# Kernel optimization log

Measured on AMD Instinct MI355X. Metric: run time of the kernel, lower is better.

Reference implementation:

```python
import jax, jax.numpy as jnp
import numpy as np
import math

B, TQ, TK = 64, 1024, 512
CONV_CH, EMBED_DIM, ATT_HID = 512, 512, 512
KEY_POS_RATE = 1.385
QUERY_POS_RATE = 1.0
POSITION_WEIGHT = 1.0


def sin_pos_enc(positions, w, d):
    # positions: [B, T] int, padding_idx=0 maps to zero vector.
    # pe[..., 2i]   = sin(w*pos / 10000^(2i/d))
    # pe[..., 2i+1] = cos(w*pos / 10000^(2i/d))
    i = jnp.arange(d)
    inv_freq = jnp.power(jnp.float32(10000.0), -(2.0 * (i // 2).astype(jnp.float32)) / d)  # [d]
    ang = (positions.astype(jnp.float32) * w)[..., None] * inv_freq  # [B, T, d]
    pe = jnp.where(i % 2 == 0, jnp.sin(ang), jnp.cos(ang))
    return jnp.where((positions == 0)[..., None], jnp.float32(0.0), pe)


def setup_inputs() -> dict:
    key = jax.random.key(0)
    ks = jax.random.split(key, 12)
    s = 0.02
    inp = {
        "query": jax.random.normal(ks[0], (B, TQ, CONV_CH), jnp.float32),
        "keys": jax.random.normal(ks[1], (B, TK, EMBED_DIM), jnp.float32),
        "values": jax.random.normal(ks[2], (B, TK, EMBED_DIM), jnp.float32),
        # 1-based positions (0 is the padding index of SinusoidalEncoding)
        "text_positions": jnp.broadcast_to(jnp.arange(1, TK + 1, dtype=jnp.int64), (B, TK)),
        "frame_positions": jnp.broadcast_to(jnp.arange(1, TQ + 1, dtype=jnp.int64), (B, TQ)),
        # pad mask over keys: last 64 text positions are padding
        "mask": jnp.broadcast_to(jnp.arange(TK) >= (TK - 64), (B, TK)),
        "Wq": jax.random.normal(ks[3], (CONV_CH, ATT_HID), jnp.float32) * s,
        "bq": jnp.zeros((ATT_HID,), jnp.float32),
        "Wk": jax.random.normal(ks[4], (EMBED_DIM, ATT_HID), jnp.float32) * s,
        "bk": jnp.zeros((ATT_HID,), jnp.float32),
        "Wv": jax.random.normal(ks[5], (EMBED_DIM, ATT_HID), jnp.float32) * s,
        "bv": jnp.zeros((ATT_HID,), jnp.float32),
        "Wo": jax.random.normal(ks[6], (ATT_HID, CONV_CH), jnp.float32) * s,
        "bo": jnp.zeros((CONV_CH,), jnp.float32),
    }
    return inp


def reference(query, keys, values, text_positions, frame_positions, mask,
              Wq, bq, Wk, bk, Wv, bv, Wo, bo):
    # positional-bias injection (position_weight = 1.0)
    keys = keys + POSITION_WEIGHT * sin_pos_enc(text_positions, KEY_POS_RATE, EMBED_DIM)[:, :keys.shape[1], :]
    query = query + POSITION_WEIGHT * sin_pos_enc(frame_positions, QUERY_POS_RATE, CONV_CH)[:, :frame_positions.shape[-1], :]

    v = values @ Wv + bv            # [B, TK, H]
    k = keys @ Wk + bk              # [B, TK, H]
    q = query @ Wq + bq             # [B, TQ, H]

    scores = jnp.einsum('bqh,bkh->bqk', q, k)               # [B, TQ, TK]
    scores = jnp.where(mask[:, None, :], -jnp.inf, scores)
    attn = jax.nn.softmax(scores, axis=2)
    # dropout is a no-op in eval mode
    x = jnp.einsum('bqk,bkh->bqh', attn, v)
    x = x * jnp.float32(math.sqrt(1.0 / v.shape[1]))
    out = x @ Wo + bo               # [B, TQ, conv_channels]
    return out, attn
```

## Files before the change

### kernel.cpp

```cpp
#include <hip/hip_runtime.h>
#include <stdint.h>

#define DEVI __device__ __forceinline__

typedef __attribute__((ext_vector_type(4))) float     f4v;
typedef __attribute__((ext_vector_type(8))) _Float16  h8;
typedef __attribute__((ext_vector_type(4))) _Float16  h4;
typedef unsigned int  u32;

static constexpr int   TQ = 1024, TKN = 512;
static constexpr float KEY_RATE = 1.385f;
static constexpr float QRY_RATE = 1.0f;
static constexpr float SCALE    = 0.04419417382415922f;
static constexpr float INVC     = 0.05190512648261504f;

static constexpr size_t OFF_MM   = 0;
static constexpr size_t OFF_NT   = OFF_MM  + (size_t)512*512*2;
static constexpr size_t OFF_WOT  = OFF_NT  + (size_t)512*512*2;
static constexpr size_t OFF_PEQ  = OFF_WOT + (size_t)512*512*4;
static constexpr size_t OFF_W    = OFF_PEQ + (size_t)1024*512*4;
static constexpr size_t OFF_C    = OFF_W   + 512*4;
static constexpr size_t OFF_BQBK = OFF_C   + 512*4;
static constexpr size_t OFF_T    = OFF_BQBK + 256;
static constexpr size_t OFF_KP   = OFF_T   + (size_t)64*512*4;
static constexpr size_t OFF_MKT  = OFF_KP  + (size_t)64*512*512*2;
static constexpr size_t OFF_PT   = OFF_MKT + (size_t)64*512*512*2;
static constexpr size_t WS_NEED  = OFF_PT  + (size_t)64*512*512*2;
static constexpr size_t OFF_A16  = WS_NEED;
static constexpr size_t WS_BIG   = OFF_A16 + (size_t)64*1024*512*2;

DEVI f4v mfma16(h8 a, h8 b, f4v c) {
  return __builtin_amdgcn_mfma_f32_16x16x32_f16(a, b, c, 0, 0, 0);
}

DEVI void gld16(void* lds, const void* g) {
  __builtin_amdgcn_global_load_lds(
      (const __attribute__((address_space(1))) unsigned int*)g,
      (__attribute__((address_space(3))) unsigned int*)lds, 16, 0, 0);
}

DEVI void stage_B(char* Bbuf, const _Float16* B, int k0, int tid) {
#pragma unroll
  for (int it = 0; it < 4; ++it) {
    const int c = (it << 9) + tid;
    const int r = c >> 2, s = c & 3;
    const int sg = s ^ ((r >> 1) & 3);
    gld16(Bbuf + ((size_t)c << 4), B + (size_t)r * 512 + k0 + (sg << 3));
  }
}

DEVI void stage_A16(char* Abuf, const _Float16* A, int k0, int tid) {
  const int r = tid >> 2, s = tid & 3;
  const int sg = s ^ ((r >> 1) & 3);
  gld16(Abuf + ((size_t)tid << 4), A + (size_t)r * 512 + k0 + (sg << 3));
}

DEVI void loads_A32(f4v& x0, f4v& x1, const float* A, const float* add, int k0, int tid) {
  const int r = tid >> 2, c8 = (tid & 3) << 3;
  const float* p = A + (size_t)r * 512 + k0 + c8;
  x0 = *(const f4v*)p; x1 = *(const f4v*)(p + 4);
  if (add) {
    const float* q = add + (size_t)r * 512 + k0 + c8;
    x0 += *(const f4v*)q; x1 += *(const f4v*)(q + 4);
  }
}
DEVI void write_A32(char* Abuf, f4v x0, f4v x1, int tid) {
  const int r = tid >> 2;
  const int slot = (tid & 3) ^ ((r >> 1) & 3);
  h8 o;
#pragma unroll
  for (int i = 0; i < 4; ++i) { o[i] = (_Float16)x0[i]; o[4 + i] = (_Float16)x1[i]; }
  *(h8*)(Abuf + (r << 6) + (slot << 4)) = o;
}

DEVI void read_frags(const char* Ab, const char* Bb, int wr, int wc, int lane,
                     h8 (&a)[4], h8 (&b)[8]) {
  const int l15 = lane & 15, hi = lane >> 4;
#pragma unroll
  for (int mi = 0; mi < 4; ++mi) {
    const int r = wr * 64 + mi * 16 + l15;
    a[mi] = *(const h8*)(Ab + (r << 6) + ((hi ^ ((r >> 1) & 3)) << 4));
  }
#pragma unroll
  for (int nj = 0; nj < 8; ++nj) {
    const int g = wc * 128 + nj * 16 + l15;
    b[nj] = *(const h8*)(Bb + (g << 6) + ((hi ^ ((g >> 1) & 3)) << 4));
  }
}

#define MFMA_ALL(a, bf, acc)                                   \
  _Pragma("unroll") for (int mi = 0; mi < 4; ++mi)             \
  _Pragma("unroll") for (int nj = 0; nj < 8; ++nj)             \
      acc[mi][nj] = mfma16(a[mi], bf[nj], acc[mi][nj]);

DEVI void stage_f32_A(char* Abuf, const float* A, int k0, int tid) {
#pragma unroll
  for (int it = 0; it < 2; ++it) {
    const int idx = (it << 9) + tid;
    const int r = idx >> 3, c4 = idx & 7;
    f4v x = *(const f4v*)(A + (size_t)r * 512 + k0 + (c4 << 2));
    h4 o;
#pragma unroll
    for (int i = 0; i < 4; ++i) o[i] = (_Float16)x[i];
    const int slot = (c4 >> 1) ^ ((r >> 1) & 3);
    *(h4*)(Abuf + (r << 6) + (slot << 4) + ((c4 & 1) << 3)) = o;
  }
}
DEVI void stage_f32_B(char* Bbuf, const float* B, int k0, int tid) {
#pragma unroll
  for (int it = 0; it < 8; ++it) {
    const int idx = (it << 9) + tid;
    const int r = idx >> 3, c4 = idx & 7;
    f4v x = *(const f4v*)(B + (size_t)r * 512 + k0 + (c4 << 2));
    h4 o;
#pragma unroll
    for (int i = 0; i < 4; ++i) o[i] = (_Float16)x[i];
    const int slot = (c4 >> 1) ^ ((r >> 1) & 3);
    *(h4*)(Bbuf + (r << 6) + (slot << 4) + ((c4 & 1) << 3)) = o;
  }
}

__global__ __launch_bounds__(512) void k_prep_small(
    const float* __restrict__ Wk, const float* __restrict__ bq,
    const float* __restrict__ bk, const float* __restrict__ bv,
    const float* __restrict__ Wo, const float* __restrict__ bo,
    float* __restrict__ wvec, float* __restrict__ cvec, float* __restrict__ bqbk) {
  __shared__ float red[512];
  const int tid = threadIdx.x, wid = tid >> 6, lane = tid & 63;
  if (blockIdx.x < 64) {
    const int row = blockIdx.x * 8 + wid;
    const float* p = Wk + (size_t)row * 512 + lane * 8;
    const f4v a = *(const f4v*)p, c = *(const f4v*)(p + 4);
    const f4v b0 = *(const f4v*)(bq + lane * 8), b1 = *(const f4v*)(bq + lane * 8 + 4);
    float d = a[0]*b0[0]+a[1]*b0[1]+a[2]*b0[2]+a[3]*b0[3]
            + c[0]*b1[0]+c[1]*b1[1]+c[2]*b1[2]+c[3]*b1[3];
#pragma unroll
    for (int off = 32; off; off >>= 1) d += __shfl_xor(d, off);
    if (lane == 0) wvec[row] = d;
  } else {
    float acc = 0.f;
    for (int a = 0; a < 512; ++a) acc += bv[a] * Wo[(size_t)a * 512 + tid];
    cvec[tid] = SCALE * acc + bo[tid];
    red[tid] = bq[tid] * bk[tid];
    __syncthreads();
    if (tid == 0) { float s = 0.f; for (int h = 0; h < 512; ++h) s += red[h]; bqbk[0] = s; }
  }
}

__global__ void k_prep_peq(const void* __restrict__ fpos_raw, float* __restrict__ PEQ) {
  const u32* fp = (const u32*)fpos_raw;
  const bool is64 = (fp[1] == 0);
  const int t  = blockIdx.x * 256 + threadIdx.x;
  const int tq = t >> 9, d = t & 511;
  const int pos = (int)(is64 ? fp[2 * tq] : fp[tq]);
  float pe = 0.f;
  if (pos != 0) {
    const float invf = exp2f(-(float)(d >> 1) * INVC);
    const float ang  = ((float)pos * QRY_RATE) * invf;
    pe = (d & 1) ? cosf(ang) : sinf(ang);
  }
  PEQ[t] = pe;
}

__global__ __launch_bounds__(256) void k_wo_t(const float* __restrict__ Wo,
                                              float* __restrict__ WoT) {
  __shared__ float t[32][33];
  const int tx = threadIdx.x, ty = threadIdx.y;
  const int x = blockIdx.x * 32 + tx;
#pragma unroll
  for (int j = 0; j < 4; ++j)
    t[ty + 8 * j][tx] = Wo[(size_t)(blockIdx.y * 32 + ty + 8 * j) * 512 + x];
  __syncthreads();
  const int x2 = blockIdx.y * 32 + tx;
#pragma unroll
  for (int j = 0; j < 4; ++j)
    WoT[(size_t)(blockIdx.x * 32 + ty + 8 * j) * 512 + x2] = t[tx][ty + 8 * j];
}

__global__ __launch_bounds__(512) void k_prep_mats(
    const float* __restrict__ Wq, const float* __restrict__ Wk,
    const float* __restrict__ WoT, const float* __restrict__ Wv,
    _Float16* __restrict__ Mm, _Float16* __restrict__ Nt) {
  __shared__ char lds[40960];
  char *Ab = lds, *Bb = lds + 8192;
  const int tid = threadIdx.x, lane = tid & 63, wid = tid >> 6;
  const int wr = wid >> 2, wc = wid & 3;
  const float* A = (blockIdx.y == 0 ? Wq : WoT) + (size_t)blockIdx.x * 128 * 512;
  const float* B = (blockIdx.y == 0 ? Wk : Wv);
  _Float16* out = (blockIdx.y == 0 ? Mm : Nt) + (size_t)blockIdx.x * 128 * 512;
  f4v acc[4][8] = {};
  for (int ks = 0; ks < 16; ++ks) {
    stage_f32_A(Ab, A, ks * 32, tid);
    stage_f32_B(Bb, B, ks * 32, tid);
    __syncthreads();
    h8 a[4], bf[8];
    read_frags(Ab, Bb, wr, wc, lane, a, bf);
    MFMA_ALL(a, bf, acc);
    __syncthreads();
  }
  const int l15 = lane & 15, hi = lane >> 4;
#pragma unroll
  for (int mi = 0; mi < 4; ++mi)
#pragma unroll
    for (int nj = 0; nj < 8; ++nj) {
      const int col = wc * 128 + nj * 16 + l15;
#pragma unroll
      for (int j = 0; j < 4; ++j) {
        const int row = wr * 64 + mi * 16 + hi * 4 + j;
        out[(size_t)row * 512 + col] = (_Float16)acc[mi][nj][j];
      }
    }
}

__global__ __launch_bounds__(256) void k_prep_keys(
    const float* __restrict__ keys, const void* __restrict__ tpos_raw,
    const void* __restrict__ mask_raw,
    const float* __restrict__ wvec, const float* __restrict__ bqbk,
    _Float16* __restrict__ kp, float* __restrict__ tvec) {
  const u32* tp = (const u32*)tpos_raw;
  const bool is64 = (tp[1] == 0);
  const int tid = threadIdx.x, wid = tid >> 6, lane = tid & 63;
  const int row = blockIdx.x * 4 + wid;
  const int pos = (int)(is64 ? tp[2 * row] : tp[row]);
  const int d0  = lane * 8;
  const float* src = keys + (size_t)row * 512 + d0;
  const f4v a = *(const f4v*)src, b = *(const f4v*)(src + 4);
  float x[8] = {a[0], a[1], a[2], a[3], b[0], b[1], b[2], b[3]};
  if (pos != 0) {
    const float pw = (float)pos * KEY_RATE;
#pragma unroll
    for (int u = 0; u < 4; ++u) {
      const float invf = exp2f(-(float)(lane * 4 + u) * INVC);
      const float ang  = pw * invf;
      x[2*u]   += sinf(ang);
      x[2*u+1] += cosf(ang);
    }
  }
  const f4v w0 = *(const f4v*)(wvec + d0), w1 = *(const f4v*)(wvec + d0 + 4);
  float dot = 0.f;
#pragma unroll
  for (int i = 0; i < 4; ++i) dot += x[i] * w0[i] + x[4+i] * w1[i];
#pragma unroll
  for (int off = 32; off; off >>= 1) dot += __shfl_xor(dot, off);
  if (lane == 0) {
    const u32* m32 = (const u32*)mask_raw;
    const bool is32 = (m32[448] != 0);
    const bool mk = is32 ? (m32[row] != 0)
                         : (((const unsigned char*)mask_raw)[row] != 0);
    tvec[row] = mk ? -1e30f : (dot + bqbk[0]);
  }
  h8 o;
#pragma unroll
  for (int i = 0; i < 8; ++i) o[i] = (_Float16)x[i];
  *(h8*)(kp + (size_t)row * 512 + d0) = o;
}


__global__ __launch_bounds__(512, 2) void k_mk(
    const _Float16* __restrict__ kp, const _Float16* __restrict__ Mm,
    _Float16* __restrict__ MKt) {
  __shared__ char lds[81920];
  char *Ac = lds, *An = lds + 8192, *Bc = lds + 16384, *Bn = lds + 49152;
  const int tid = threadIdx.x, lane = tid & 63, wid = tid >> 6;
  const int wr = wid >> 2, wc = wid & 3;
  const int tt = blockIdx.x, b = blockIdx.y;
  const _Float16* As = kp + ((size_t)b * TKN + tt * 128) * 512;
  f4v acc[4][8] = {};
  stage_A16(Ac, As, 0, tid);
  stage_B(Bc, Mm, 0, tid);
  __syncthreads();
  for (int ks = 0; ks < 16; ++ks) {
    if (ks < 15) { stage_A16(An, As, (ks + 1) * 32, tid); stage_B(Bn, Mm, (ks + 1) * 32, tid); }
    h8 a[4], bf[8];
    read_frags(Ac, Bc, wr, wc, lane, a, bf);
    MFMA_ALL(a, bf, acc);
    __syncthreads();
    char* t = Ac; Ac = An; An = t; t = Bc; Bc = Bn; Bn = t;
  }
  _Float16* Ob = MKt + (size_t)b * TKN * 512 + (size_t)tt * 128 * 512;
  const int l15 = lane & 15, hi = lane >> 4;
#pragma unroll
  for (int mi = 0; mi < 4; ++mi)
#pragma unroll
    for (int nj = 0; nj < 8; ++nj) {
      const int col = wc * 128 + nj * 16 + l15;
#pragma unroll
      for (int j = 0; j < 4; ++j) {
        const int row = wr * 64 + mi * 16 + hi * 4 + j;
        Ob[(size_t)row * 512 + col] = (_Float16)acc[mi][nj][j];
      }
    }
}

__global__ __launch_bounds__(512, 2) void k_scores(
    const float* __restrict__ query, const float* __restrict__ PEQ,
    const _Float16* __restrict__ MKt, const float* __restrict__ tve,
    float* __restrict__ attn, _Float16* __restrict__ a16) {
  __shared__ char lds[81920];
  char *Ac = lds, *An = lds + 8192, *Bc = lds + 16384, *Bn = lds + 49152;
  const int tid = threadIdx.x, lane = tid & 63, wid = tid >> 6;
  const int wr = wid >> 2, wc = wid & 3;
  const int qt = blockIdx.x, b = blockIdx.y;
  const float* As = query + ((size_t)b * TQ + qt * 128) * 512;
  const float* Ad = PEQ + (size_t)(qt * 128) * 512;
  const _Float16* Bs = MKt + (size_t)b * TKN * 512;
  const int l15 = lane & 15, hi = lane >> 4;
  float tv[8];
#pragma unroll
  for (int nj = 0; nj < 8; ++nj) tv[nj] = tve[b * TKN + wc * 128 + nj * 16 + l15];
  f4v acc[4][8] = {};
  f4v x0, x1;
  loads_A32(x0, x1, As, Ad, 0, tid);
  stage_B(Bc, Bs, 0, tid);
  write_A32(Ac, x0, x1, tid);
  __syncthreads();
  for (int ks = 0; ks < 16; ++ks) {
    if (ks < 15) { loads_A32(x0, x1, As, Ad, (ks + 1) * 32, tid); stage_B(Bn, Bs, (ks + 1) * 32, tid); }
    h8 a[4], bf[8];
    read_frags(Ac, Bc, wr, wc, lane, a, bf);
    MFMA_ALL(a, bf, acc);
    if (ks < 15) write_A32(An, x0, x1, tid);
    __syncthreads();
    char* t = Ac; Ac = An; An = t; t = Bc; Bc = Bn; Bn = t;
  }
  float* red  = (float*)lds;
  float* red2 = (float*)(lds + 2048);
#pragma unroll
  for (int mi = 0; mi < 4; ++mi)
#pragma unroll
    for (int nj = 0; nj < 8; ++nj) {
      const float t = tv[nj];
#pragma unroll
      for (int j = 0; j < 4; ++j) acc[mi][nj][j] += t;
    }
  float mrow[4][4];
#pragma unroll
  for (int mi = 0; mi < 4; ++mi)
#pragma unroll
    for (int j = 0; j < 4; ++j) {
      float m = acc[mi][0][j];
#pragma unroll
      for (int nj = 1; nj < 8; ++nj) m = fmaxf(m, acc[mi][nj][j]);
      m = fmaxf(m, __shfl_xor(m, 1)); m = fmaxf(m, __shfl_xor(m, 2));
      m = fmaxf(m, __shfl_xor(m, 4)); m = fmaxf(m, __shfl_xor(m, 8));
      mrow[mi][j] = m;
    }
  if (l15 == 0) {
#pragma unroll
    for (int mi = 0; mi < 4; ++mi)
#pragma unroll
      for (int j = 0; j < 4; ++j)
        red[(wr * 64 + mi * 16 + hi * 4 + j) * 4 + wc] = mrow[mi][j];
  }
  __syncthreads();
#pragma unroll
  for (int mi = 0; mi < 4; ++mi)
#pragma unroll
    for (int j = 0; j < 4; ++j) {
      const f4v rv = *(const f4v*)(red + (wr * 64 + mi * 16 + hi * 4 + j) * 4);
      mrow[mi][j] = fmaxf(fmaxf(rv[0], rv[1]), fmaxf(rv[2], rv[3]));
    }
  float srow[4][4];
#pragma unroll
  for (int mi = 0; mi < 4; ++mi)
#pragma unroll
    for (int j = 0; j < 4; ++j) {
      float s = 0.f;
      const float m = mrow[mi][j];
#pragma unroll
      for (int nj = 0; nj < 8; ++nj) {
        const float e = expf(acc[mi][nj][j] - m);
        acc[mi][nj][j] = e; s += e;
      }
      s += __shfl_xor(s, 1); s += __shfl_xor(s, 2);
      s += __shfl_xor(s, 4); s += __shfl_xor(s, 8);
      srow[mi][j] = s;
    }
  if (l15 == 0) {
#pragma unroll
    for (int mi = 0; mi < 4; ++mi)
#pragma unroll
      for (int j = 0; j < 4; ++j)
        red2[(wr * 64 + mi * 16 + hi * 4 + j) * 4 + wc] = srow[mi][j];
  }
  __syncthreads();
  float* Ao = attn + ((size_t)b * TQ + qt * 128) * 512;
  _Float16* Ah = a16 ? a16 + ((size_t)b * TQ + qt * 128) * 512 : nullptr;
#pragma unroll
  for (int mi = 0; mi < 4; ++mi)
#pragma unroll
    for (int j = 0; j < 4; ++j) {
      const int row = wr * 64 + mi * 16 + hi * 4 + j;
      const f4v sv = *(const f4v*)(red2 + row * 4);
      const float rinv = 1.f / (sv[0] + sv[1] + sv[2] + sv[3]);
#pragma unroll
      for (int nj = 0; nj < 8; ++nj) {
        const float v = acc[mi][nj][j] * rinv;
        const int col = wc * 128 + nj * 16 + l15;
        Ao[(size_t)row * 512 + col] = v;
        if (Ah) Ah[(size_t)row * 512 + col] = (_Float16)v;
      }
    }
}

__global__ __launch_bounds__(512, 2) void k_pv(
    const float* __restrict__ values, const _Float16* __restrict__ Nt,
    _Float16* __restrict__ Pt) {
  __shared__ char lds[81920];
  char *Ac = lds, *An = lds + 8192, *Bc = lds + 16384, *Bn = lds + 49152;
  const int tid = threadIdx.x, lane = tid & 63, wid = tid >> 6;
  const int wr = wid >> 2, wc = wid & 3;
  const int rt = blockIdx.x, b = blockIdx.y;
  const float* As = values + ((size_t)b * TKN + rt * 128) * 512;
  f4v acc[4][8] = {};
  f4v x0, x1;
  loads_A32(x0, x1, As, nullptr, 0, tid);
  stage_B(Bc, Nt, 0, tid);
  write_A32(Ac, x0, x1, tid);
  __syncthreads();
  for (int ks = 0; ks < 16; ++ks) {
    if (ks < 15) { loads_A32(x0, x1, As, nullptr, (ks + 1) * 32, tid); stage_B(Bn, Nt, (ks + 1) * 32, tid); }
    h8 a[4], bf[8];
    read_frags(Ac, Bc, wr, wc, lane, a, bf);
    MFMA_ALL(a, bf, acc);
    if (ks < 15) write_A32(An, x0, x1, tid);
    __syncthreads();
    char* t = Ac; Ac = An; An = t; t = Bc; Bc = Bn; Bn = t;
  }
  const int l15 = lane & 15, hi = lane >> 4;
  _Float16* Pb = Pt + (size_t)b * 512 * 512;
#pragma unroll
  for (int mi = 0; mi < 4; ++mi)
#pragma unroll
    for (int nj = 0; nj < 8; ++nj) {
      const int col = wc * 128 + nj * 16 + l15;
      const int t0  = rt * 128 + wr * 64 + mi * 16 + hi * 4;
      h4 o;
#pragma unroll
      for (int j = 0; j < 4; ++j) o[j] = (_Float16)acc[mi][nj][j];
      *(h4*)(Pb + (size_t)col * 512 + t0) = o;
    }
}

template <int A16P>
__global__ __launch_bounds__(512, 2) void k_final(
    const float* __restrict__ attn, const _Float16* __restrict__ attn16,
    const _Float16* __restrict__ Pt, const float* __restrict__ cvec,
    float* __restrict__ outp) {
  __shared__ char lds[81920];
  char *Ac = lds, *An = lds + 8192, *Bc = lds + 16384, *Bn = lds + 49152;
  const int tid = threadIdx.x, lane = tid & 63, wid = tid >> 6;
  const int wr = wid >> 2, wc = wid & 3;
  const int qt = blockIdx.x, b = blockIdx.y;
  const float* As = attn + ((size_t)b * TQ + qt * 128) * 512;
  const _Float16* As16 = attn16 + ((size_t)b * TQ + qt * 128) * 512;
  const _Float16* Bs = Pt + (size_t)b * 512 * 512;
  const int l15 = lane & 15, hi = lane >> 4;
  float cv[8];
#pragma unroll
  for (int nj = 0; nj < 8; ++nj) cv[nj] = cvec[wc * 128 + nj * 16 + l15];
  f4v acc[4][8] = {};
  f4v x0, x1;
  if (A16P) {
    stage_A16(Ac, As16, 0, tid);
  } else {
    loads_A32(x0, x1, As, nullptr, 0, tid);
  }
  stage_B(Bc, Bs, 0, tid);
  if (!A16P) write_A32(Ac, x0, x1, tid);
  __syncthreads();
  for (int ks = 0; ks < 16; ++ks) {
    if (ks < 15) {
      if (A16P) stage_A16(An, As16, (ks + 1) * 32, tid);
      else      loads_A32(x0, x1, As, nullptr, (ks + 1) * 32, tid);
      stage_B(Bn, Bs, (ks + 1) * 32, tid);
    }
    h8 a[4], bf[8];
    read_frags(Ac, Bc, wr, wc, lane, a, bf);
    MFMA_ALL(a, bf, acc);
    if (!A16P && ks < 15) write_A32(An, x0, x1, tid);
    __syncthreads();
    char* t = Ac; Ac = An; An = t; t = Bc; Bc = Bn; Bn = t;
  }
  float* Ob = outp + ((size_t)b * TQ + qt * 128) * 512;
#pragma unroll
  for (int mi = 0; mi < 4; ++mi)
#pragma unroll
    for (int nj = 0; nj < 8; ++nj) {
      const int col = wc * 128 + nj * 16 + l15;
#pragma unroll
      for (int j = 0; j < 4; ++j) {
        const int row = wr * 64 + mi * 16 + hi * 4 + j;
        Ob[(size_t)row * 512 + col] = SCALE * acc[mi][nj][j] + cv[nj];
      }
    }
}

extern "C" void kernel_launch(void* const* d_in, const int* in_sizes, int n_in,
                              void* d_out, int out_size, void* d_ws, size_t ws_size,
                              hipStream_t stream) {
  (void)in_sizes; (void)n_in; (void)out_size;
  if (ws_size < WS_NEED) return;
  const bool big = (ws_size >= WS_BIG);

  const float* query  = (const float*)d_in[0];
  const float* keys   = (const float*)d_in[1];
  const float* values = (const float*)d_in[2];
  const void*  tpos   = d_in[3];
  const void*  fpos   = d_in[4];
  const void*  mask   = d_in[5];
  const float* Wq = (const float*)d_in[6];
  const float* bq = (const float*)d_in[7];
  const float* Wk = (const float*)d_in[8];
  const float* bk = (const float*)d_in[9];
  const float* Wv = (const float*)d_in[10];
  const float* bv = (const float*)d_in[11];
  const float* Wo = (const float*)d_in[12];
  const float* bo = (const float*)d_in[13];

  char* ws = (char*)d_ws;
  _Float16* Mm   = (_Float16*)(ws + OFF_MM);
  _Float16* Nt   = (_Float16*)(ws + OFF_NT);
  float*    WoT  = (float*)   (ws + OFF_WOT);
  float*    PEQ  = (float*)   (ws + OFF_PEQ);
  float*    wvec = (float*)   (ws + OFF_W);
  float*    cvec = (float*)   (ws + OFF_C);
  float*    bqbk = (float*)   (ws + OFF_BQBK);
  float*    tvec = (float*)   (ws + OFF_T);
  _Float16* kp   = (_Float16*)(ws + OFF_KP);
  _Float16* MKt  = (_Float16*)(ws + OFF_MKT);
  _Float16* Pt   = (_Float16*)(ws + OFF_PT);
  _Float16* a16  = big ? (_Float16*)(ws + OFF_A16) : nullptr;

  float* outp = (float*)d_out;
  float* attn = outp + (size_t)64 * TQ * 512;

  k_prep_small<<<65, 512, 0, stream>>>(Wk, bq, bk, bv, Wo, bo, wvec, cvec, bqbk);
  k_prep_peq  <<<2048, 256, 0, stream>>>(fpos, PEQ);
  k_wo_t      <<<dim3(16, 16), dim3(32, 8), 0, stream>>>(Wo, WoT);
  k_prep_mats <<<dim3(4, 2), 512, 0, stream>>>(Wq, Wk, WoT, Wv, Mm, Nt);
  k_prep_keys <<<8192, 256, 0, stream>>>(keys, tpos, mask, wvec, bqbk, kp, tvec);
  k_mk        <<<dim3(4, 64), 512, 0, stream>>>(kp, Mm, MKt);
  k_scores    <<<dim3(8, 64), 512, 0, stream>>>(query, PEQ, MKt, tvec, attn, a16);
  k_pv        <<<dim3(4, 64), 512, 0, stream>>>(values, Nt, Pt);
  if (big) k_final<1><<<dim3(8, 64), 512, 0, stream>>>(attn, a16, Pt, cvec, outp);
  else     k_final<0><<<dim3(8, 64), 512, 0, stream>>>(attn, a16, Pt, cvec, outp);
}
```

Measured before the change: 359.6 us.

## Fuse softmax and PV into one attention kernel, merge prep launches

Merges the scores kernel with the final attn@P GEMM so the normalized probabilities are kept in registers, written to LDS as fp16, and multiplied by Pt in the same block. This removes the re-read of the fp32 attention matrix (or its fp16 copy) from global memory and the separate final launch. It also collapses the small prep kernels into two launches, merges the MK and PV GEMMs into one grid, and maps blocks to batches with an XCD-aware interleave. The cost is higher LDS use per block (96KB), which may cut occupancy, plus serialized per-column-tile writes of P into LDS with extra barriers.

```diff
diff --git a/kernel.cpp b/kernel.cpp
--- a/kernel.cpp
+++ b/kernel.cpp
@@ -26,8 +26,6 @@
 static constexpr size_t OFF_MKT  = OFF_KP  + (size_t)64*512*512*2;
 static constexpr size_t OFF_PT   = OFF_MKT + (size_t)64*512*512*2;
 static constexpr size_t WS_NEED  = OFF_PT  + (size_t)64*512*512*2;
-static constexpr size_t OFF_A16  = WS_NEED;
-static constexpr size_t WS_BIG   = OFF_A16 + (size_t)64*1024*512*2;
 
 DEVI f4v mfma16(h8 a, h8 b, f4v c) {
   return __builtin_amdgcn_mfma_f32_16x16x32_f16(a, b, c, 0, 0, 0);
@@ -73,18 +71,28 @@
   *(h8*)(Abuf + (r << 6) + (slot << 4)) = o;
 }
 
-DEVI void read_frags(const char* Ab, const char* Bb, int wr, int wc, int lane,
-                     h8 (&a)[4], h8 (&b)[8]) {
+DEVI void read_fragsA(const char* Ab, int wr, int lane, h8 (&a)[4]) {
   const int l15 = lane & 15, hi = lane >> 4;
 #pragma unroll
   for (int mi = 0; mi < 4; ++mi) {
     const int r = wr * 64 + mi * 16 + l15;
     a[mi] = *(const h8*)(Ab + (r << 6) + ((hi ^ ((r >> 1) & 3)) << 4));
   }
+}
+DEVI void read_fragsB(const char* Bb, int wc, int lane, h8 (&b)[8]) {
+  const int l15 = lane & 15, hi = lane >> 4;
 #pragma unroll
   for (int nj = 0; nj < 8; ++nj) {
     const int g = wc * 128 + nj * 16 + l15;
     b[nj] = *(const h8*)(Bb + (g << 6) + ((hi ^ ((g >> 1) & 3)) << 4));
+  }
+}
+DEVI void read_fragsP(const char* Pb, int kt, int wr, int lane, h8 (&a)[4]) {
+  const int l15 = lane & 15, hi = lane >> 4;
+#pragma unroll
+  for (int mi = 0; mi < 4; ++mi) {
+    const int r = wr * 64 + mi * 16 + l15;
+    a[mi] = *(const h8*)(Pb + r * 256 + (kt << 6) + ((hi ^ ((r >> 1) & 3)) << 4));
   }
 }
 
@@ -120,15 +128,17 @@
   }
 }
 
-__global__ __launch_bounds__(512) void k_prep_small(
+__global__ __launch_bounds__(256) void k_prepA(
     const float* __restrict__ Wk, const float* __restrict__ bq,
     const float* __restrict__ bk, const float* __restrict__ bv,
     const float* __restrict__ Wo, const float* __restrict__ bo,
-    float* __restrict__ wvec, float* __restrict__ cvec, float* __restrict__ bqbk) {
-  __shared__ float red[512];
-  const int tid = threadIdx.x, wid = tid >> 6, lane = tid & 63;
-  if (blockIdx.x < 64) {
-    const int row = blockIdx.x * 8 + wid;
+    const void* __restrict__ fpos_raw,
+    float* __restrict__ wvec, float* __restrict__ cvec, float* __restrict__ bqbk,
+    float* __restrict__ PEQ, float* __restrict__ WoT) {
+  const int bid = blockIdx.x, tid = threadIdx.x;
+  if (bid < 128) {
+    const int wid = tid >> 6, lane = tid & 63;
+    const int row = bid * 4 + wid;
     const float* p = Wk + (size_t)row * 512 + lane * 8;
     const f4v a = *(const f4v*)p, c = *(const f4v*)(p + 4);
     const f4v b0 = *(const f4v*)(bq + lane * 8), b1 = *(const f4v*)(bq + lane * 8 + 4);
@@ -137,194 +147,241 @@
 #pragma unroll
     for (int off = 32; off; off >>= 1) d += __shfl_xor(d, off);
     if (lane == 0) wvec[row] = d;
+  } else if (bid == 128) {
+    __shared__ float red[256];
+#pragma unroll
+    for (int u = 0; u < 2; ++u) {
+      const int i = tid + u * 256;
+      float acc = 0.f;
+      for (int a = 0; a < 512; ++a) acc += bv[a] * Wo[(size_t)a * 512 + i];
+      cvec[i] = SCALE * acc + bo[i];
+    }
+    red[tid] = bq[tid] * bk[tid] + bq[tid + 256] * bk[tid + 256];
+    __syncthreads();
+    if (tid == 0) { float s = 0.f; for (int h = 0; h < 256; ++h) s += red[h]; bqbk[0] = s; }
+  } else if (bid < 129 + 2048) {
+    const u32* fp = (const u32*)fpos_raw;
+    const bool is64 = (fp[1] == 0);
+    const int t = (bid - 129) * 256 + tid;
+    const int tq = t >> 9, d = t & 511;
+    const int pos = (int)(is64 ? fp[2 * tq] : fp[tq]);
+    float pe = 0.f;
+    if (pos != 0) {
+      const float invf = exp2f(-(float)(d >> 1) * INVC);
+      const float ang  = ((float)pos * QRY_RATE) * invf;
+      pe = (d & 1) ? cosf(ang) : sinf(ang);
+    }
+    PEQ[t] = pe;
   } else {
-    float acc = 0.f;
-    for (int a = 0; a < 512; ++a) acc += bv[a] * Wo[(size_t)a * 512 + tid];
-    cvec[tid] = SCALE * acc + bo[tid];
-    red[tid] = bq[tid] * bk[tid];
-    __syncthreads();
-    if (tid == 0) { float s = 0.f; for (int h = 0; h < 512; ++h) s += red[h]; bqbk[0] = s; }
-  }
-}
-
-__global__ void k_prep_peq(const void* __restrict__ fpos_raw, float* __restrict__ PEQ) {
-  const u32* fp = (const u32*)fpos_raw;
-  const bool is64 = (fp[1] == 0);
-  const int t  = blockIdx.x * 256 + threadIdx.x;
-  const int tq = t >> 9, d = t & 511;
-  const int pos = (int)(is64 ? fp[2 * tq] : fp[tq]);
-  float pe = 0.f;
-  if (pos != 0) {
-    const float invf = exp2f(-(float)(d >> 1) * INVC);
-    const float ang  = ((float)pos * QRY_RATE) * invf;
-    pe = (d & 1) ? cosf(ang) : sinf(ang);
-  }
-  PEQ[t] = pe;
-}
-
-__global__ __launch_bounds__(256) void k_wo_t(const float* __restrict__ Wo,
-                                              float* __restrict__ WoT) {
-  __shared__ float t[32][33];
-  const int tx = threadIdx.x, ty = threadIdx.y;
-  const int x = blockIdx.x * 32 + tx;
-#pragma unroll
-  for (int j = 0; j < 4; ++j)
-    t[ty + 8 * j][tx] = Wo[(size_t)(blockIdx.y * 32 + ty + 8 * j) * 512 + x];
-  __syncthreads();
-  const int x2 = blockIdx.y * 32 + tx;
-#pragma unroll
-  for (int j = 0; j < 4; ++j)
-    WoT[(size_t)(blockIdx.x * 32 + ty + 8 * j) * 512 + x2] = t[tx][ty + 8 * j];
-}
-
-__global__ __launch_bounds__(512) void k_prep_mats(
+    __shared__ float t[32][33];
+    const int local = bid - 2177;
+    const int bx = local & 15, by = local >> 4;
+    const int tx = tid & 31, ty = tid >> 5;
+    const int x = bx * 32 + tx;
+#pragma unroll
+    for (int j = 0; j < 4; ++j)
+      t[ty + 8 * j][tx] = Wo[(size_t)(by * 32 + ty + 8 * j) * 512 + x];
+    __syncthreads();
+    const int x2 = by * 32 + tx;
+#pragma unroll
+    for (int j = 0; j < 4; ++j)
+      WoT[(size_t)(bx * 32 + ty + 8 * j) * 512 + x2] = t[tx][ty + 8 * j];
+  }
+}
+
+__global__ __launch_bounds__(512) void k_prepB(
     const float* __restrict__ Wq, const float* __restrict__ Wk,
     const float* __restrict__ WoT, const float* __restrict__ Wv,
-    _Float16* __restrict__ Mm, _Float16* __restrict__ Nt) {
-  __shared__ char lds[40960];
-  char *Ab = lds, *Bb = lds + 8192;
-  const int tid = threadIdx.x, lane = tid & 63, wid = tid >> 6;
-  const int wr = wid >> 2, wc = wid & 3;
-  const float* A = (blockIdx.y == 0 ? Wq : WoT) + (size_t)blockIdx.x * 128 * 512;
-  const float* B = (blockIdx.y == 0 ? Wk : Wv);
-  _Float16* out = (blockIdx.y == 0 ? Mm : Nt) + (size_t)blockIdx.x * 128 * 512;
-  f4v acc[4][8] = {};
-  for (int ks = 0; ks < 16; ++ks) {
-    stage_f32_A(Ab, A, ks * 32, tid);
-    stage_f32_B(Bb, B, ks * 32, tid);
-    __syncthreads();
-    h8 a[4], bf[8];
-    read_frags(Ab, Bb, wr, wc, lane, a, bf);
-    MFMA_ALL(a, bf, acc);
-    __syncthreads();
-  }
-  const int l15 = lane & 15, hi = lane >> 4;
-#pragma unroll
-  for (int mi = 0; mi < 4; ++mi)
-#pragma unroll
-    for (int nj = 0; nj < 8; ++nj) {
-      const int col = wc * 128 + nj * 16 + l15;
-#pragma unroll
-      for (int j = 0; j < 4; ++j) {
-        const int row = wr * 64 + mi * 16 + hi * 4 + j;
-        out[(size_t)row * 512 + col] = (_Float16)acc[mi][nj][j];
-      }
-    }
-}
-
-__global__ __launch_bounds__(256) void k_prep_keys(
     const float* __restrict__ keys, const void* __restrict__ tpos_raw,
     const void* __restrict__ mask_raw,
     const float* __restrict__ wvec, const float* __restrict__ bqbk,
+    _Float16* __restrict__ Mm, _Float16* __restrict__ Nt,
     _Float16* __restrict__ kp, float* __restrict__ tvec) {
-  const u32* tp = (const u32*)tpos_raw;
-  const bool is64 = (tp[1] == 0);
-  const int tid = threadIdx.x, wid = tid >> 6, lane = tid & 63;
-  const int row = blockIdx.x * 4 + wid;
-  const int pos = (int)(is64 ? tp[2 * row] : tp[row]);
-  const int d0  = lane * 8;
-  const float* src = keys + (size_t)row * 512 + d0;
-  const f4v a = *(const f4v*)src, b = *(const f4v*)(src + 4);
-  float x[8] = {a[0], a[1], a[2], a[3], b[0], b[1], b[2], b[3]};
-  if (pos != 0) {
-    const float pw = (float)pos * KEY_RATE;
-#pragma unroll
-    for (int u = 0; u < 4; ++u) {
-      const float invf = exp2f(-(float)(lane * 4 + u) * INVC);
-      const float ang  = pw * invf;
-      x[2*u]   += sinf(ang);
-      x[2*u+1] += cosf(ang);
-    }
-  }
-  const f4v w0 = *(const f4v*)(wvec + d0), w1 = *(const f4v*)(wvec + d0 + 4);
-  float dot = 0.f;
-#pragma unroll
-  for (int i = 0; i < 4; ++i) dot += x[i] * w0[i] + x[4+i] * w1[i];
-#pragma unroll
-  for (int off = 32; off; off >>= 1) dot += __shfl_xor(dot, off);
-  if (lane == 0) {
-    const u32* m32 = (const u32*)mask_raw;
-    const bool is32 = (m32[448] != 0);
-    const bool mk = is32 ? (m32[row] != 0)
-                         : (((const unsigned char*)mask_raw)[row] != 0);
-    tvec[row] = mk ? -1e30f : (dot + bqbk[0]);
-  }
-  h8 o;
-#pragma unroll
-  for (int i = 0; i < 8; ++i) o[i] = (_Float16)x[i];
-  *(h8*)(kp + (size_t)row * 512 + d0) = o;
-}
-
-
-__global__ __launch_bounds__(512, 2) void k_mk(
+  __shared__ char lds[40960];
+  const int bid = blockIdx.x, tid = threadIdx.x;
+  const int lane = tid & 63, wid = tid >> 6;
+  if (bid < 8) {
+    char *Ab = lds, *Bb = lds + 8192;
+    const int wr = wid >> 2, wc = wid & 3;
+    const int x = bid & 3, y = bid >> 2;
+    const float* A = (y == 0 ? Wq : WoT) + (size_t)x * 128 * 512;
+    const float* B = (y == 0 ? Wk : Wv);
+    _Float16* out = (y == 0 ? Mm : Nt) + (size_t)x * 128 * 512;
+    f4v acc[4][8] = {};
+    for (int ks = 0; ks < 16; ++ks) {
+      stage_f32_A(Ab, A, ks * 32, tid);
+      stage_f32_B(Bb, B, ks * 32, tid);
+      __syncthreads();
+      h8 a[4], bf[8];
+      read_fragsA(Ab, wr, lane, a);
+      read_fragsB(Bb, wc, lane, bf);
+      MFMA_ALL(a, bf, acc);
+      __syncthreads();
+    }
+    const int l15 = lane & 15, hi = lane >> 4;
+#pragma unroll
+    for (int mi = 0; mi < 4; ++mi)
+#pragma unroll
+      for (int nj = 0; nj < 8; ++nj) {
+        const int col = wc * 128 + nj * 16 + l15;
+#pragma unroll
+        for (int j = 0; j < 4; ++j) {
+          const int row = wr * 64 + mi * 16 + hi * 4 + j;
+          out[(size_t)row * 512 + col] = (_Float16)acc[mi][nj][j];
+        }
+      }
+  } else {
+    const u32* tp = (const u32*)tpos_raw;
+    const bool is64 = (tp[1] == 0);
+    const int row = (bid - 8) * 8 + wid;
+    const int pos = (int)(is64 ? tp[2 * row] : tp[row]);
+    const int d0  = lane * 8;
+    const float* src = keys + (size_t)row * 512 + d0;
+    const f4v a = *(const f4v*)src, b = *(const f4v*)(src + 4);
+    float x[8] = {a[0], a[1], a[2], a[3], b[0], b[1], b[2], b[3]};
+    if (pos != 0) {
+      const float pw = (float)pos * KEY_RATE;
+#pragma unroll
+      for (int u = 0; u < 4; ++u) {
+        const float invf = exp2f(-(float)(lane * 4 + u) * INVC);
+        const float ang  = pw * invf;
+        x[2*u]   += sinf(ang);
+        x[2*u+1] += cosf(ang);
+      }
+    }
+    const f4v w0 = *(const f4v*)(wvec + d0), w1 = *(const f4v*)(wvec + d0 + 4);
+    float dot = 0.f;
+#pragma unroll
+    for (int i = 0; i < 4; ++i) dot += x[i] * w0[i] + x[4+i] * w1[i];
+#pragma unroll
+    for (int off = 32; off; off >>= 1) dot += __shfl_xor(dot, off);
+    if (lane == 0) {
+      const u32* m32 = (const u32*)mask_raw;
+      const bool is32 = (m32[448] != 0);
+      const bool mk = is32 ? (m32[row] != 0)
+                           : (((const unsigned char*)mask_raw)[row] != 0);
+      tvec[row] = mk ? -1e30f : (dot + bqbk[0]);
+    }
+    h8 o;
+#pragma unroll
+    for (int i = 0; i < 8; ++i) o[i] = (_Float16)x[i];
+    *(h8*)(kp + (size_t)row * 512 + d0) = o;
+  }
+}
+
+__global__ __launch_bounds__(512, 2) void k_mkpv(
     const _Float16* __restrict__ kp, const _Float16* __restrict__ Mm,
-    _Float16* __restrict__ MKt) {
+    const float* __restrict__ values, const _Float16* __restrict__ Nt,
+    _Float16* __restrict__ MKt, _Float16* __restrict__ Pt) {
   __shared__ char lds[81920];
   char *Ac = lds, *An = lds + 8192, *Bc = lds + 16384, *Bn = lds + 49152;
+  const int bid = blockIdx.x, tid = threadIdx.x;
+  const int lane = tid & 63, wid = tid >> 6;
+  const int wr = wid >> 2, wc = wid & 3;
+  const int l15 = lane & 15, hi = lane >> 4;
+  f4v acc[4][8] = {};
+  if (bid < 256) {
+    const int tt = bid & 3, b = bid >> 2;
+    const _Float16* As = kp + ((size_t)b * TKN + tt * 128) * 512;
+    stage_A16(Ac, As, 0, tid);
+    stage_B(Bc, Mm, 0, tid);
+    __syncthreads();
+    for (int ks = 0; ks < 16; ++ks) {
+      if (ks < 15) { stage_A16(An, As, (ks + 1) * 32, tid); stage_B(Bn, Mm, (ks + 1) * 32, tid); }
+      h8 a[4], bf[8];
+      read_fragsA(Ac, wr, lane, a);
+      read_fragsB(Bc, wc, lane, bf);
+      MFMA_ALL(a, bf, acc);
+      __syncthreads();
+      char* t = Ac; Ac = An; An = t; t = Bc; Bc = Bn; Bn = t;
+    }
+    _Float16* Ob = MKt + (size_t)b * TKN * 512 + (size_t)tt * 128 * 512;
+#pragma unroll
+    for (int mi = 0; mi < 4; ++mi)
+#pragma unroll
+      for (int nj = 0; nj < 8; ++nj) {
+        const int col = wc * 128 + nj * 16 + l15;
+#pragma unroll
+        for (int j = 0; j < 4; ++j) {
+          const int row = wr * 64 + mi * 16 + hi * 4 + j;
+          Ob[(size_t)row * 512 + col] = (_Float16)acc[mi][nj][j];
+        }
+      }
+  } else {
+    const int rt = (bid - 256) & 3, b = (bid - 256) >> 2;
+    const float* As = values + ((size_t)b * TKN + rt * 128) * 512;
+    f4v x0, x1;
+    loads_A32(x0, x1, As, nullptr, 0, tid);
+    stage_B(Bc, Nt, 0, tid);
+    write_A32(Ac, x0, x1, tid);
+    __syncthreads();
+    for (int ks = 0; ks < 16; ++ks) {
+      if (ks < 15) { loads_A32(x0, x1, As, nullptr, (ks + 1) * 32, tid); stage_B(Bn, Nt, (ks + 1) * 32, tid); }
+      h8 a[4], bf[8];
+      read_fragsA(Ac, wr, lane, a);
+      read_fragsB(Bc, wc, lane, bf);
+      MFMA_ALL(a, bf, acc);
+      if (ks < 15) write_A32(An, x0, x1, tid);
+      __syncthreads();
+      char* t = Ac; Ac = An; An = t; t = Bc; Bc = Bn; Bn = t;
+    }
+    _Float16* Pb = Pt + (size_t)b * 512 * 512;
+#pragma unroll
+    for (int mi = 0; mi < 4; ++mi)
+#pragma unroll
+      for (int nj = 0; nj < 8; ++nj) {
+        const int col = wc * 128 + nj * 16 + l15;
+        const int t0  = rt * 128 + wr * 64 + mi * 16 + hi * 4;
+        h4 o;
+#pragma unroll
+        for (int j = 0; j < 4; ++j) o[j] = (_Float16)acc[mi][nj][j];
+        *(h4*)(Pb + (size_t)col * 512 + t0) = o;
+      }
+  }
+}
+
+__global__ __launch_bounds__(512, 2) void k_att(
+    const float* __restrict__ query, const float* __restrict__ PEQ,
+    const _Float16* __restrict__ MKt, const float* __restrict__ tve,
+    const _Float16* __restrict__ Pt, const float* __restrict__ cvec,
+    float* __restrict__ attn, float* __restrict__ outp) {
+  __shared__ char lds[98304];
+  char *A0 = lds, *A1 = lds + 8192, *B0 = lds + 16384, *B1 = lds + 49152;
+  float* red  = (float*)(lds + 81920);
+  float* red2 = (float*)(lds + 83968);
+  const int bid = blockIdx.x;
+  const int xcd = bid & 7, jj = bid >> 3;
+  const int b = xcd + 8 * (jj & 7), qt = jj >> 3;
   const int tid = threadIdx.x, lane = tid & 63, wid = tid >> 6;
   const int wr = wid >> 2, wc = wid & 3;
-  const int tt = blockIdx.x, b = blockIdx.y;
-  const _Float16* As = kp + ((size_t)b * TKN + tt * 128) * 512;
-  f4v acc[4][8] = {};
-  stage_A16(Ac, As, 0, tid);
-  stage_B(Bc, Mm, 0, tid);
-  __syncthreads();
-  for (int ks = 0; ks < 16; ++ks) {
-    if (ks < 15) { stage_A16(An, As, (ks + 1) * 32, tid); stage_B(Bn, Mm, (ks + 1) * 32, tid); }
-    h8 a[4], bf[8];
-    read_frags(Ac, Bc, wr, wc, lane, a, bf);
-    MFMA_ALL(a, bf, acc);
-    __syncthreads();
-    char* t = Ac; Ac = An; An = t; t = Bc; Bc = Bn; Bn = t;
-  }
-  _Float16* Ob = MKt + (size_t)b * TKN * 512 + (size_t)tt * 128 * 512;
   const int l15 = lane & 15, hi = lane >> 4;
-#pragma unroll
-  for (int mi = 0; mi < 4; ++mi)
-#pragma unroll
-    for (int nj = 0; nj < 8; ++nj) {
-      const int col = wc * 128 + nj * 16 + l15;
-#pragma unroll
-      for (int j = 0; j < 4; ++j) {
-        const int row = wr * 64 + mi * 16 + hi * 4 + j;
-        Ob[(size_t)row * 512 + col] = (_Float16)acc[mi][nj][j];
-      }
-    }
-}
-
-__global__ __launch_bounds__(512, 2) void k_scores(
-    const float* __restrict__ query, const float* __restrict__ PEQ,
-    const _Float16* __restrict__ MKt, const float* __restrict__ tve,
-    float* __restrict__ attn, _Float16* __restrict__ a16) {
-  __shared__ char lds[81920];
-  char *Ac = lds, *An = lds + 8192, *Bc = lds + 16384, *Bn = lds + 49152;
-  const int tid = threadIdx.x, lane = tid & 63, wid = tid >> 6;
-  const int wr = wid >> 2, wc = wid & 3;
-  const int qt = blockIdx.x, b = blockIdx.y;
   const float* As = query + ((size_t)b * TQ + qt * 128) * 512;
   const float* Ad = PEQ + (size_t)(qt * 128) * 512;
   const _Float16* Bs = MKt + (size_t)b * TKN * 512;
-  const int l15 = lane & 15, hi = lane >> 4;
+  const _Float16* PtB = Pt + (size_t)b * 512 * 512;
   float tv[8];
 #pragma unroll
   for (int nj = 0; nj < 8; ++nj) tv[nj] = tve[b * TKN + wc * 128 + nj * 16 + l15];
+
   f4v acc[4][8] = {};
   f4v x0, x1;
   loads_A32(x0, x1, As, Ad, 0, tid);
-  stage_B(Bc, Bs, 0, tid);
-  write_A32(Ac, x0, x1, tid);
+  stage_B(B0, Bs, 0, tid);
+  write_A32(A0, x0, x1, tid);
   __syncthreads();
+  char *Ac = A0, *An = A1, *Bc = B0, *Bn = B1;
   for (int ks = 0; ks < 16; ++ks) {
     if (ks < 15) { loads_A32(x0, x1, As, Ad, (ks + 1) * 32, tid); stage_B(Bn, Bs, (ks + 1) * 32, tid); }
     h8 a[4], bf[8];
-    read_frags(Ac, Bc, wr, wc, lane, a, bf);
+    read_fragsA(Ac, wr, lane, a);
+    read_fragsB(Bc, wc, lane, bf);
     MFMA_ALL(a, bf, acc);
     if (ks < 15) write_A32(An, x0, x1, tid);
     __syncthreads();
     char* t = Ac; Ac = An; An = t; t = Bc; Bc = Bn; Bn = t;
   }
-  float* red  = (float*)lds;
-  float* red2 = (float*)(lds + 2048);
+  stage_B(lds + 32768, PtB, 0, tid);
+
 #pragma unroll
   for (int mi = 0; mi < 4; ++mi)
 #pragma unroll
@@ -384,8 +441,9 @@
         red2[(wr * 64 + mi * 16 + hi * 4 + j) * 4 + wc] = srow[mi][j];
   }
   __syncthreads();
+
   float* Ao = attn + ((size_t)b * TQ + qt * 128) * 512;
-  _Float16* Ah = a16 ? a16 + ((size_t)b * TQ + qt * 128) * 512 : nullptr;
+  h4 pk[4][8];
 #pragma unroll
   for (int mi = 0; mi < 4; ++mi)
 #pragma unroll
@@ -396,102 +454,52 @@
 #pragma unroll
       for (int nj = 0; nj < 8; ++nj) {
         const float v = acc[mi][nj][j] * rinv;
-        const int col = wc * 128 + nj * 16 + l15;
-        Ao[(size_t)row * 512 + col] = v;
-        if (Ah) Ah[(size_t)row * 512 + col] = (_Float16)v;
-      }
-    }
-}
-
-__global__ __launch_bounds__(512, 2) void k_pv(
-    const float* __restrict__ values, const _Float16* __restrict__ Nt,
-    _Float16* __restrict__ Pt) {
-  __shared__ char lds[81920];
-  char *Ac = lds, *An = lds + 8192, *Bc = lds + 16384, *Bn = lds + 49152;
-  const int tid = threadIdx.x, lane = tid & 63, wid = tid >> 6;
-  const int wr = wid >> 2, wc = wid & 3;
-  const int rt = blockIdx.x, b = blockIdx.y;
-  const float* As = values + ((size_t)b * TKN + rt * 128) * 512;
-  f4v acc[4][8] = {};
-  f4v x0, x1;
-  loads_A32(x0, x1, As, nullptr, 0, tid);
-  stage_B(Bc, Nt, 0, tid);
-  write_A32(Ac, x0, x1, tid);
-  __syncthreads();
-  for (int ks = 0; ks < 16; ++ks) {
-    if (ks < 15) { loads_A32(x0, x1, As, nullptr, (ks + 1) * 32, tid); stage_B(Bn, Nt, (ks + 1) * 32, tid); }
-    h8 a[4], bf[8];
-    read_frags(Ac, Bc, wr, wc, lane, a, bf);
-    MFMA_ALL(a, bf, acc);
-    if (ks < 15) write_A32(An, x0, x1, tid);
-    __syncthreads();
-    char* t = Ac; Ac = An; An = t; t = Bc; Bc = Bn; Bn = t;
-  }
-  const int l15 = lane & 15, hi = lane >> 4;
-  _Float16* Pb = Pt + (size_t)b * 512 * 512;
+        Ao[(size_t)row * 512 + wc * 128 + nj * 16 + l15] = v;
+        pk[mi][nj][j] = (_Float16)v;
+      }
+    }
+
+  f4v oacc[4][8] = {};
+  char* Pl = lds;
+  for (int ct = 0; ct < 4; ++ct) {
+    __syncthreads();
+    if (wc == ct) {
+#pragma unroll
+      for (int mi = 0; mi < 4; ++mi)
+#pragma unroll
+        for (int nj = 0; nj < 8; ++nj)
+#pragma unroll
+          for (int j = 0; j < 4; ++j) {
+            const int r = wr * 64 + mi * 16 + hi * 4 + j;
+            const int cc = (((nj & 1) << 1) | (l15 >> 3)) ^ ((r >> 1) & 3);
+            *(_Float16*)(Pl + r * 256 + ((nj >> 1) << 6) + (cc << 4) + ((l15 & 7) << 1)) =
+                pk[mi][nj][j];
+          }
+    }
+    __syncthreads();
+    for (int kt = 0; kt < 4; ++kt) {
+      const int s = ct * 4 + kt;
+      if (s < 15) stage_B(lds + 32768 + (((s + 1) & 1) << 15), PtB, (s + 1) * 32, tid);
+      h8 a[4], bb[8];
+      read_fragsP(Pl, kt, wr, lane, a);
+      read_fragsB(lds + 32768 + ((s & 1) << 15), wc, lane, bb);
+      MFMA_ALL(a, bb, oacc);
+      if (kt < 3) __syncthreads();
+    }
+  }
+  float cv[8];
+#pragma unroll
+  for (int nj = 0; nj < 8; ++nj) cv[nj] = cvec[wc * 128 + nj * 16 + l15];
+  float* Ob = outp + ((size_t)b * TQ + qt * 128) * 512;
 #pragma unroll
   for (int mi = 0; mi < 4; ++mi)
 #pragma unroll
     for (int nj = 0; nj < 8; ++nj) {
       const int col = wc * 128 + nj * 16 + l15;
-      const int t0  = rt * 128 + wr * 64 + mi * 16 + hi * 4;
-      h4 o;
-#pragma unroll
-      for (int j = 0; j < 4; ++j) o[j] = (_Float16)acc[mi][nj][j];
-      *(h4*)(Pb + (size_t)col * 512 + t0) = o;
-    }
-}
-
-template <int A16P>
-__global__ __launch_bounds__(512, 2) void k_final(
-    const float* __restrict__ attn, const _Float16* __restrict__ attn16,
-    const _Float16* __restrict__ Pt, const float* __restrict__ cvec,
-    float* __restrict__ outp) {
-  __shared__ char lds[81920];
-  char *Ac = lds, *An = lds + 8192, *Bc = lds + 16384, *Bn = lds + 49152;
-  const int tid = threadIdx.x, lane = tid & 63, wid = tid >> 6;
-  const int wr = wid >> 2, wc = wid & 3;
-  const int qt = blockIdx.x, b = blockIdx.y;
-  const float* As = attn + ((size_t)b * TQ + qt * 128) * 512;
-  const _Float16* As16 = attn16 + ((size_t)b * TQ + qt * 128) * 512;
-  const _Float16* Bs = Pt + (size_t)b * 512 * 512;
-  const int l15 = lane & 15, hi = lane >> 4;
-  float cv[8];
-#pragma unroll
-  for (int nj = 0; nj < 8; ++nj) cv[nj] = cvec[wc * 128 + nj * 16 + l15];
-  f4v acc[4][8] = {};
-  f4v x0, x1;
-  if (A16P) {
-    stage_A16(Ac, As16, 0, tid);
-  } else {
-    loads_A32(x0, x1, As, nullptr, 0, tid);
-  }
-  stage_B(Bc, Bs, 0, tid);
-  if (!A16P) write_A32(Ac, x0, x1, tid);
-  __syncthreads();
-  for (int ks = 0; ks < 16; ++ks) {
-    if (ks < 15) {
-      if (A16P) stage_A16(An, As16, (ks + 1) * 32, tid);
-      else      loads_A32(x0, x1, As, nullptr, (ks + 1) * 32, tid);
-      stage_B(Bn, Bs, (ks + 1) * 32, tid);
-    }
-    h8 a[4], bf[8];
-    read_frags(Ac, Bc, wr, wc, lane, a, bf);
-    MFMA_ALL(a, bf, acc);
-    if (!A16P && ks < 15) write_A32(An, x0, x1, tid);
-    __syncthreads();
-    char* t = Ac; Ac = An; An = t; t = Bc; Bc = Bn; Bn = t;
-  }
-  float* Ob = outp + ((size_t)b * TQ + qt * 128) * 512;
-#pragma unroll
-  for (int mi = 0; mi < 4; ++mi)
-#pragma unroll
-    for (int nj = 0; nj < 8; ++nj) {
-      const int col = wc * 128 + nj * 16 + l15;
 #pragma unroll
       for (int j = 0; j < 4; ++j) {
         const int row = wr * 64 + mi * 16 + hi * 4 + j;
-        Ob[(size_t)row * 512 + col] = SCALE * acc[mi][nj][j] + cv[nj];
+        Ob[(size_t)row * 512 + col] = SCALE * oacc[mi][nj][j] + cv[nj];
       }
     }
 }
@@ -501,7 +509,6 @@
                               hipStream_t stream) {
   (void)in_sizes; (void)n_in; (void)out_size;
   if (ws_size < WS_NEED) return;
-  const bool big = (ws_size >= WS_BIG);
 
   const float* query  = (const float*)d_in[0];
   const float* keys   = (const float*)d_in[1];
@@ -530,19 +537,14 @@
   _Float16* kp   = (_Float16*)(ws + OFF_KP);
   _Float16* MKt  = (_Float16*)(ws + OFF_MKT);
   _Float16* Pt   = (_Float16*)(ws + OFF_PT);
-  _Float16* a16  = big ? (_Float16*)(ws + OFF_A16) : nullptr;
 
   float* outp = (float*)d_out;
   float* attn = outp + (size_t)64 * TQ * 512;
 
-  k_prep_small<<<65, 512, 0, stream>>>(Wk, bq, bk, bv, Wo, bo, wvec, cvec, bqbk);
-  k_prep_peq  <<<2048, 256, 0, stream>>>(fpos, PEQ);
-  k_wo_t      <<<dim3(16, 16), dim3(32, 8), 0, stream>>>(Wo, WoT);
-  k_prep_mats <<<dim3(4, 2), 512, 0, stream>>>(Wq, Wk, WoT, Wv, Mm, Nt);
-  k_prep_keys <<<8192, 256, 0, stream>>>(keys, tpos, mask, wvec, bqbk, kp, tvec);
-  k_mk        <<<dim3(4, 64), 512, 0, stream>>>(kp, Mm, MKt);
-  k_scores    <<<dim3(8, 64), 512, 0, stream>>>(query, PEQ, MKt, tvec, attn, a16);
-  k_pv        <<<dim3(4, 64), 512, 0, stream>>>(values, Nt, Pt);
-  if (big) k_final<1><<<dim3(8, 64), 512, 0, stream>>>(attn, a16, Pt, cvec, outp);
-  else     k_final<0><<<dim3(8, 64), 512, 0, stream>>>(attn, a16, Pt, cvec, outp);
-}
+  k_prepA<<<2433, 256, 0, stream>>>(Wk, bq, bk, bv, Wo, bo, fpos,
+                                    wvec, cvec, bqbk, PEQ, WoT);
+  k_prepB<<<4104, 512, 0, stream>>>(Wq, Wk, WoT, Wv, keys, tpos, mask,
+                                    wvec, bqbk, Mm, Nt, kp, tvec);
+  k_mkpv <<<512, 512, 0, stream>>>(kp, Mm, values, Nt, MKt, Pt);
+  k_att  <<<512, 512, 0, stream>>>(query, PEQ, MKt, tvec, Pt, cvec, attn, outp);
+}
```

Result: slower. 662.7 us (+84.3%).
